# Kernel tuning notes

Hardware: AMD Instinct MI355X
Metric: run time of the kernel (lower is better)

The kernel has to match this reference:

```python
import jax, jax.numpy as jnp
import numpy as np

KEY_DIM = 64
SCALE_PER_SEQ = 1.0 / np.sqrt(KEY_DIM).astype(np.float32)   # attn_scale_factor_per_seq default
SCALE_OVER_SEQS = 1.0 / np.sqrt(KEY_DIM).astype(np.float32) # attn_scale_factor_over_seqs default


def setup_inputs() -> dict:
    key = jax.random.key(0)
    ks = jax.random.split(key, 6)
    b, i, t, j, d = 8, 256, 64, 256, 256
    kd, vd = KEY_DIM, 64
    return {
        "input_seq": jax.random.normal(ks[0], (b, i, d), dtype=jnp.float32),
        "memory_x": jax.random.normal(ks[1], (b, t, j, d), dtype=jnp.float32),
        "memory_y": jax.random.normal(ks[2], (b, t, j, d), dtype=jnp.float32),
        "Wq": jax.random.normal(ks[3], (d, kd), dtype=jnp.float32) * (1.0 / np.sqrt(d)),
        "bq": jnp.zeros((kd,), dtype=jnp.float32),
        "Wk": jax.random.normal(ks[4], (d, kd), dtype=jnp.float32) * (1.0 / np.sqrt(d)),
        "bk": jnp.zeros((kd,), dtype=jnp.float32),
        "Wv": jax.random.normal(ks[5], (d, vd), dtype=jnp.float32) * (1.0 / np.sqrt(d)),
        "bv": jnp.zeros((vd,), dtype=jnp.float32),
    }


def reference(input_seq, memory_x, memory_y, Wq, bq, Wk, bk, Wv, bv):
    # Dense projections
    queries = input_seq @ Wq + bq            # [b, i, kd]
    keys = memory_x @ Wk + bk                # [b, t, j, kd]
    values = memory_y @ Wv + bv              # [b, t, j, vd]

    # Raw scores between every query and every token of every memory sequence
    attn_mat = jnp.einsum('bik,btjk->btij', queries, keys)  # [b, t, i, j]

    # Level 1: within-sequence attention (softmax over tokens j)
    per_seq_attn = jax.nn.softmax(SCALE_PER_SEQ * attn_mat, axis=-1)
    per_seq_retrieved = jnp.einsum('btij,btjk->btik', per_seq_attn, values)  # [b, t, i, vd]

    # Level 2: over-sequences attention (max over j, softmax over t)
    mem_seq_scores = jnp.max(attn_mat, axis=-1)                      # [b, t, i]
    mem_seq_attn = jax.nn.softmax(SCALE_OVER_SEQS * mem_seq_scores, axis=1)

    retrieved_mems = jnp.einsum('bti,btik->bik', mem_seq_attn, per_seq_retrieved)  # [b, i, vd]
    return retrieved_mems
```

## Files before the change

kernel.cpp:

```cpp
#include <hip/hip_runtime.h>
#include <hip/hip_bf16.h>

#define NB 8
#define NT 64
#define NI 256
#define NJ 256
#define ND 256
#define NKD 64
#define NVD 64
#define SCL 0.125f

typedef __attribute__((ext_vector_type(4))) float f32x4;
typedef __attribute__((ext_vector_type(8))) short bf16x8;
typedef __attribute__((ext_vector_type(4))) short bf16x4;
typedef __attribute__((ext_vector_type(4))) unsigned int uint32x4;

#define MFMA16(A, B, C) __builtin_amdgcn_mfma_f32_16x16x32_bf16((A), (B), (C), 0, 0, 0)

#define R2B 32768

__device__ __forceinline__ unsigned short f2bf(float x) {
  return __builtin_bit_cast(unsigned short, __float2bfloat16(x));
}
__device__ __forceinline__ float bf2f(unsigned short h) {
  return __builtin_bit_cast(float, (unsigned)h << 16);
}
__device__ __forceinline__ void split8(const float* __restrict__ x, bf16x8& hi, bf16x8& lo) {
  #pragma unroll
  for (int e = 0; e < 8; ++e) {
    unsigned short h = f2bf(x[e]);
    hi[e] = (short)h;
    lo[e] = (short)f2bf(x[e] - bf2f(h));
  }
}

__global__ __launch_bounds__(256) void k_prep_projq(
    const float* __restrict__ x, const float* __restrict__ Wq,
    const float* __restrict__ bq,
    const float* __restrict__ Wk, const float* __restrict__ Wv,
    unsigned short* __restrict__ Wkth, unsigned short* __restrict__ Wvth,
    unsigned short* __restrict__ Qh) {
  int tid = threadIdx.x;
  if (blockIdx.x >= 128) {
    int t0 = (blockIdx.x - 128) * 2048 + tid * 8;
    #pragma unroll
    for (int e = 0; e < 8; ++e) {
      int t = t0 + e;
      int d = t >> 6, kd = t & 63;
      Wkth[kd * 256 + d] = f2bf(Wk[t]);
      Wvth[kd * 256 + d] = f2bf(Wv[t]);
    }
    return;
  }
  __shared__ __align__(16) float wqs[256 * 64];
  __shared__ __align__(16) float xs[16 * 256];
  #pragma unroll 8
  for (int it = 0; it < 64; ++it)
    wqs[tid + it * 256] = Wq[tid + it * 256];
  int r0 = blockIdx.x * 16;
  #pragma unroll
  for (int it = 0; it < 16; ++it)
    xs[tid + it * 256] = x[(size_t)r0 * 256 + tid + it * 256];
  __syncthreads();
  int kd = tid & 63, rr = tid >> 6;
  #pragma unroll
  for (int rp = 0; rp < 4; ++rp) {
    int r = rp * 4 + rr;
    float a0 = bq[kd], a1 = 0.f, a2 = 0.f, a3 = 0.f;
    #pragma unroll 4
    for (int d = 0; d < 256; d += 4) {
      a0 = fmaf(xs[r * 256 + d],     wqs[(d)     * 64 + kd], a0);
      a1 = fmaf(xs[r * 256 + d + 1], wqs[(d + 1) * 64 + kd], a1);
      a2 = fmaf(xs[r * 256 + d + 2], wqs[(d + 2) * 64 + kd], a2);
      a3 = fmaf(xs[r * 256 + d + 3], wqs[(d + 3) * 64 + kd], a3);
    }
    Qh[(size_t)(r0 + r) * 64 + kd] = f2bf((a0 + a1) + (a2 + a3));
  }
}

__device__ __forceinline__ void stage_plane(
    char* dstb, const unsigned short* __restrict__ Wt, int tid) {
  #pragma unroll
  for (int it = 0; it < 4; ++it) {
    int qq = tid + it * 512;
    int r = qq >> 5, pb = qq & 31;
    uint4 v = *(const uint4*)((const char*)Wt + (size_t)qq * 16);
    *(uint4*)(dstb + r * 512 + ((pb ^ (r & 7)) << 4)) = v;
  }
}

__global__ __launch_bounds__(512, 4) void k_fused(
    const float* __restrict__ Xm, const float* __restrict__ Ym,
    const unsigned short* __restrict__ Wkth, const unsigned short* __restrict__ Wvth,
    const float* __restrict__ bk, const float* __restrict__ bv,
    const unsigned short* __restrict__ Qh,
    unsigned short* __restrict__ R,
    float* __restrict__ Sc) {
  __shared__ __align__(16) char smemb[65536];
  int tid = threadIdx.x;
  int bt = blockIdx.x, b = bt >> 6;
  int w = tid >> 6, lane = tid & 63, c = lane & 15, g = lane >> 4;

  const float* xr0 = Xm + (size_t)bt * 65536 + (size_t)(w * 32 + c) * 256 + g * 8;
  const float* xr1 = xr0 + 16 * 256;
  const float* yr0 = Ym + (size_t)bt * 65536 + (size_t)(w * 32 + c) * 256 + g * 8;
  const float* yr1 = yr0 + 16 * 256;

  float4 xa0 = *(const float4*)(xr0),      xa1 = *(const float4*)(xr0 + 4);
  float4 xa2 = *(const float4*)(xr1),      xa3 = *(const float4*)(xr1 + 4);
  float4 xb0 = *(const float4*)(xr0 + 32), xb1 = *(const float4*)(xr0 + 36);
  float4 xb2 = *(const float4*)(xr1 + 32), xb3 = *(const float4*)(xr1 + 36);
  float4 ya0 = *(const float4*)(yr0),      ya1 = *(const float4*)(yr0 + 4);
  float4 ya2 = *(const float4*)(yr1),      ya3 = *(const float4*)(yr1 + 4);
  float4 yb0 = *(const float4*)(yr0 + 32), yb1 = *(const float4*)(yr0 + 36);
  float4 yb2 = *(const float4*)(yr1 + 32), yb3 = *(const float4*)(yr1 + 36);

  stage_plane(smemb, Wkth, tid);
  stage_plane(smemb + R2B, Wvth, tid);
  __syncthreads();

  f32x4 kacc[4][2];
  f32x4 vacc[2][4];
  #pragma unroll
  for (int mf = 0; mf < 4; ++mf) { kacc[mf][0] = (f32x4)0.f; kacc[mf][1] = (f32x4)0.f; }
  #pragma unroll
  for (int mf = 0; mf < 2; ++mf)
    #pragma unroll
    for (int nf = 0; nf < 4; ++nf) vacc[mf][nf] = (f32x4)0.f;

  #pragma unroll
  for (int ks = 0; ks < 8; ++ks) {
    float x0[8], x1[8];
    if (ks & 1) {
      *(float4*)&x0[0] = xb0; *(float4*)&x0[4] = xb1;
      *(float4*)&x1[0] = xb2; *(float4*)&x1[4] = xb3;
      if (ks < 6) {
        xb0 = *(const float4*)(xr0 + (ks + 2) * 32);
        xb1 = *(const float4*)(xr0 + (ks + 2) * 32 + 4);
        xb2 = *(const float4*)(xr1 + (ks + 2) * 32);
        xb3 = *(const float4*)(xr1 + (ks + 2) * 32 + 4);
      }
    } else {
      *(float4*)&x0[0] = xa0; *(float4*)&x0[4] = xa1;
      *(float4*)&x1[0] = xa2; *(float4*)&x1[4] = xa3;
      if (ks < 6) {
        xa0 = *(const float4*)(xr0 + (ks + 2) * 32);
        xa1 = *(const float4*)(xr0 + (ks + 2) * 32 + 4);
        xa2 = *(const float4*)(xr1 + (ks + 2) * 32);
        xa3 = *(const float4*)(xr1 + (ks + 2) * 32 + 4);
      }
    }
    {
      bf16x8 b0h, b0l, b1h, b1l;
      split8(x0, b0h, b0l);
      split8(x1, b1h, b1l);
      #pragma unroll
      for (int mf = 0; mf < 4; ++mf) {
        int r = mf * 16 + c;
        int ba = r * 512 + (((ks * 4 + g) ^ (r & 7)) << 4);
        bf16x8 awh = *(const bf16x8*)(smemb + ba);
        kacc[mf][0] = MFMA16(awh, b0h, kacc[mf][0]);
        kacc[mf][0] = MFMA16(awh, b0l, kacc[mf][0]);
        kacc[mf][1] = MFMA16(awh, b1h, kacc[mf][1]);
        kacc[mf][1] = MFMA16(awh, b1l, kacc[mf][1]);
      }
    }
    float y0[8], y1[8];
    if (ks & 1) {
      *(float4*)&y0[0] = yb0; *(float4*)&y0[4] = yb1;
      *(float4*)&y1[0] = yb2; *(float4*)&y1[4] = yb3;
      if (ks < 6) {
        yb0 = *(const float4*)(yr0 + (ks + 2) * 32);
        yb1 = *(const float4*)(yr0 + (ks + 2) * 32 + 4);
        yb2 = *(const float4*)(yr1 + (ks + 2) * 32);
        yb3 = *(const float4*)(yr1 + (ks + 2) * 32 + 4);
      }
    } else {
      *(float4*)&y0[0] = ya0; *(float4*)&y0[4] = ya1;
      *(float4*)&y1[0] = ya2; *(float4*)&y1[4] = ya3;
      if (ks < 6) {
        ya0 = *(const float4*)(yr0 + (ks + 2) * 32);
        ya1 = *(const float4*)(yr0 + (ks + 2) * 32 + 4);
        ya2 = *(const float4*)(yr1 + (ks + 2) * 32);
        ya3 = *(const float4*)(yr1 + (ks + 2) * 32 + 4);
      }
    }
    {
      bf16x8 a0h, a0l, a1h, a1l;
      split8(y0, a0h, a0l);
      split8(y1, a1h, a1l);
      #pragma unroll
      for (int nf = 0; nf < 4; ++nf) {
        int r = nf * 16 + c;
        int ba = R2B + r * 512 + (((ks * 4 + g) ^ (r & 7)) << 4);
        bf16x8 bwh = *(const bf16x8*)(smemb + ba);
        vacc[0][nf] = MFMA16(a0h, bwh, vacc[0][nf]);
        vacc[0][nf] = MFMA16(a0l, bwh, vacc[0][nf]);
        vacc[1][nf] = MFMA16(a1h, bwh, vacc[1][nf]);
        vacc[1][nf] = MFMA16(a1l, bwh, vacc[1][nf]);
      }
    }
  }
  bf16x8 qbh[2][2];
  #pragma unroll
  for (int ks = 0; ks < 2; ++ks)
    #pragma unroll
    for (int ic = 0; ic < 2; ++ic) {
      size_t qo = ((size_t)b * NI + w * 32 + ic * 16 + c) * NKD + ks * 32 + g * 8;
      qbh[ks][ic] = *(const bf16x8*)(Qh + qo);
    }
  __syncthreads();

  #pragma unroll
  for (int nf = 0; nf < 2; ++nf) {
    int j = w * 32 + nf * 16 + c;
    #pragma unroll
    for (int mf = 0; mf < 4; ++mf) {
      bf16x4 ph;
      #pragma unroll
      for (int r = 0; r < 4; ++r)
        ph[r] = (short)f2bf(kacc[mf][nf][r] + bk[mf * 16 + g * 4 + r]);
      int pb = mf * 2 + (g >> 1);
      int ba = j * 128 + ((pb ^ (j & 7)) << 4) + (g & 1) * 8;
      *(bf16x4*)(smemb + ba) = ph;
    }
  }
  #pragma unroll
  for (int nf = 0; nf < 4; ++nf) {
    int vd = nf * 16 + c;
    float bs = bv[vd];
    #pragma unroll
    for (int mf = 0; mf < 2; ++mf) {
      bf16x4 ph;
      #pragma unroll
      for (int r = 0; r < 4; ++r) ph[r] = (short)f2bf(vacc[mf][nf][r] + bs);
      int pb = w * 4 + mf * 2 + (g >> 1);
      int ba = R2B + vd * 512 + ((pb ^ (vd & 7)) << 4) + (g & 1) * 8;
      *(bf16x4*)(smemb + ba) = ph;
    }
  }
  __syncthreads();

  #pragma unroll
  for (int ic = 0; ic < 2; ++ic) {
    int i = w * 32 + ic * 16 + c;

    f32x4 sa[16];
    #pragma unroll
    for (int jf = 0; jf < 16; ++jf) sa[jf] = (f32x4)0.f;
    #pragma unroll
    for (int jf = 0; jf < 16; ++jf) {
      int j = jf * 16 + c;
      #pragma unroll
      for (int ks = 0; ks < 2; ++ks) {
        int ba = j * 128 + (((ks * 4 + g) ^ (j & 7)) << 4);
        bf16x8 kh = *(const bf16x8*)(smemb + ba);
        sa[jf] = MFMA16(kh, qbh[ks][ic], sa[jf]);
      }
    }

    float mx = sa[0][0];
    #pragma unroll
    for (int jf = 0; jf < 16; ++jf)
      #pragma unroll
      for (int r = 0; r < 4; ++r) mx = fmaxf(mx, sa[jf][r]);
    mx = fmaxf(mx, __shfl_xor(mx, 16));
    mx = fmaxf(mx, __shfl_xor(mx, 32));
    if (g == 0) Sc[(size_t)bt * NI + i] = mx;
    float sum = 0.f;
    #pragma unroll
    for (int jf = 0; jf < 16; ++jf)
      #pragma unroll
      for (int r = 0; r < 4; ++r) {
        float p = __expf((sa[jf][r] - mx) * SCL);
        sa[jf][r] = p;
        sum += p;
      }
    sum += __shfl_xor(sum, 16);
    sum += __shfl_xor(sum, 32);
    float linv = 1.0f / sum;

    unsigned int plo[16], phi[16];
    #pragma unroll
    for (int jf = 0; jf < 16; ++jf) {
      plo[jf] = (unsigned int)f2bf(sa[jf][0]) | ((unsigned int)f2bf(sa[jf][1]) << 16);
      phi[jf] = (unsigned int)f2bf(sa[jf][2]) | ((unsigned int)f2bf(sa[jf][3]) << 16);
    }

    int srcA = c + 32 * (g & 1);
    int srcB = srcA + 16;
    bool hiH = (g >= 2);

    f32x4 racc[4];
    #pragma unroll
    for (int vf = 0; vf < 4; ++vf) racc[vf] = (f32x4)0.f;
    #pragma unroll
    for (int js = 0; js < 8; ++js) {
      int a0 = __shfl((int)plo[2 * js], srcA);
      int a1 = __shfl((int)phi[2 * js], srcA);
      int a2 = __shfl((int)plo[2 * js], srcB);
      int a3 = __shfl((int)phi[2 * js], srcB);
      int b0 = __shfl((int)plo[2 * js + 1], srcA);
      int b1 = __shfl((int)phi[2 * js + 1], srcA);
      int b2 = __shfl((int)plo[2 * js + 1], srcB);
      int b3 = __shfl((int)phi[2 * js + 1], srcB);
      uint32x4 pw;
      pw[0] = (unsigned int)(hiH ? b0 : a0);
      pw[1] = (unsigned int)(hiH ? b1 : a1);
      pw[2] = (unsigned int)(hiH ? b2 : a2);
      pw[3] = (unsigned int)(hiH ? b3 : a3);
      bf16x8 pf = __builtin_bit_cast(bf16x8, pw);
      #pragma unroll
      for (int vf = 0; vf < 4; ++vf) {
        int vd = vf * 16 + c;
        int vba = R2B + vd * 512 + (((js * 4 + g) ^ (vd & 7)) << 4);
        bf16x8 vh = *(const bf16x8*)(smemb + vba);
        racc[vf] = MFMA16(vh, pf, racc[vf]);
      }
    }

    #pragma unroll
    for (int vf = 0; vf < 4; ++vf) {
      bf16x4 rk;
      #pragma unroll
      for (int r = 0; r < 4; ++r) rk[r] = (short)f2bf(racc[vf][r] * linv);
      *(bf16x4*)(R + ((size_t)bt * NI + i) * NKD + vf * 16 + g * 4) = rk;
    }
  }
}

__global__ __launch_bounds__(256) void k_level2(
    const float* __restrict__ Sc,
    const unsigned short* __restrict__ R,
    float* __restrict__ out) {
  int w = threadIdx.x >> 6, lane = threadIdx.x & 63;
  int bi = blockIdx.x * 4 + w;
  int b = bi >> 8, i = bi & 255;
  float sc = Sc[((size_t)b * NT + lane) * NI + i];
  float mx = sc;
  #pragma unroll
  for (int off = 32; off; off >>= 1) mx = fmaxf(mx, __shfl_xor(mx, off));
  float e = __expf((sc - mx) * SCL);
  float sum = e;
  #pragma unroll
  for (int off = 32; off; off >>= 1) sum += __shfl_xor(sum, off);
  float wn = e / sum;
  float acc = 0.f;
  for (int t = 0; t < NT; ++t) {
    float wt = __shfl(wn, t);
    acc = fmaf(wt, bf2f(R[(((size_t)b * NT + t) * NI + i) * NKD + lane]), acc);
  }
  out[((size_t)b * NI + i) * NVD + lane] = acc;
}

extern "C" void kernel_launch(void* const* d_in, const int* in_sizes, int n_in,
                              void* d_out, int out_size, void* d_ws, size_t ws_size,
                              hipStream_t stream) {
  const float* x   = (const float*)d_in[0];
  const float* mxp = (const float*)d_in[1];
  const float* myp = (const float*)d_in[2];
  const float* Wq  = (const float*)d_in[3];
  const float* bq  = (const float*)d_in[4];
  const float* Wk  = (const float*)d_in[5];
  const float* bk  = (const float*)d_in[6];
  const float* Wv  = (const float*)d_in[7];
  const float* bv  = (const float*)d_in[8];
  float* out = (float*)d_out;

  char* p = (char*)d_ws;
  auto alloc = [&](size_t bytes) { char* r = p; p += (bytes + 255) & ~(size_t)255; return r; };
  unsigned short* Qh   = (unsigned short*)alloc(2048 * 64 * 2);
  unsigned short* Rw   = (unsigned short*)alloc((size_t)131072 * 64 * 2);
  float*          Scw  = (float*)alloc((size_t)131072 * 4);
  unsigned short* Wkth = (unsigned short*)alloc(64 * 256 * 2);
  unsigned short* Wvth = (unsigned short*)alloc(64 * 256 * 2);

  hipLaunchKernelGGL(k_prep_projq, dim3(136), dim3(256), 0, stream,
                     x, Wq, bq, Wk, Wv, Wkth, Wvth, Qh);
  hipLaunchKernelGGL(k_fused, dim3(NB * NT), dim3(512), 0, stream,
                     mxp, myp, Wkth, Wvth, bk, bv, Qh, Rw, Scw);
  hipLaunchKernelGGL(k_level2, dim3(512), dim3(256), 0, stream, Scw, Rw, out);
}
```

Before: 88.90 us.

## Transpose R layout to [b,i,t,vd] and vectorize level-2 reduction over t

The fused kernel now writes the per-sequence retrieved vectors in a [b, i, t, vd] layout, so all 64 memory sequences for one query row sit next to each other. The level-2 kernel splits each wave into 8 groups over t that each load 16-byte vectors, accumulate 8 outputs, and combine the partial sums with xor shuffles. This replaces 64 serial strided scalar loads per lane with a few wide contiguous loads. In exchange, the fused kernel's stores become scattered across t, which may hurt its write coalescing.

```diff
diff --git a/kernel.cpp b/kernel.cpp
--- a/kernel.cpp
+++ b/kernel.cpp
@@ -98,7 +98,7 @@
     float* __restrict__ Sc) {
   __shared__ __align__(16) char smemb[65536];
   int tid = threadIdx.x;
-  int bt = blockIdx.x, b = bt >> 6;
+  int bt = blockIdx.x, b = bt >> 6, tmem = bt & 63;
   int w = tid >> 6, lane = tid & 63, c = lane & 15, g = lane >> 4;
 
   const float* xr0 = Xm + (size_t)bt * 65536 + (size_t)(w * 32 + c) * 256 + g * 8;
@@ -324,7 +324,7 @@
       bf16x4 rk;
       #pragma unroll
       for (int r = 0; r < 4; ++r) rk[r] = (short)f2bf(racc[vf][r] * linv);
-      *(bf16x4*)(R + ((size_t)bt * NI + i) * NKD + vf * 16 + g * 4) = rk;
+      *(bf16x4*)(R + (((size_t)b * NI + i) * NT + tmem) * NKD + vf * 16 + g * 4) = rk;
     }
   }
 }
@@ -345,12 +345,33 @@
   #pragma unroll
   for (int off = 32; off; off >>= 1) sum += __shfl_xor(sum, off);
   float wn = e / sum;
-  float acc = 0.f;
-  for (int t = 0; t < NT; ++t) {
+  int tg = lane >> 3, vg = lane & 7;
+  const unsigned short* rb = R + ((size_t)b * NI + i) * (NT * NKD);
+  float acc[8];
+  #pragma unroll
+  for (int v8 = 0; v8 < 8; ++v8) acc[v8] = 0.f;
+  #pragma unroll
+  for (int tt = 0; tt < 8; ++tt) {
+    int t = tg * 8 + tt;
     float wt = __shfl(wn, t);
-    acc = fmaf(wt, bf2f(R[(((size_t)b * NT + t) * NI + i) * NKD + lane]), acc);
-  }
-  out[((size_t)b * NI + i) * NVD + lane] = acc;
+    uint4 rv = *(const uint4*)(rb + (size_t)t * NKD + vg * 8);
+    const unsigned short* rs = (const unsigned short*)&rv;
+    #pragma unroll
+    for (int v8 = 0; v8 < 8; ++v8) acc[v8] = fmaf(wt, bf2f(rs[v8]), acc[v8]);
+  }
+  #pragma unroll
+  for (int v8 = 0; v8 < 8; ++v8) {
+    float v = acc[v8];
+    v += __shfl_xor(v, 8);
+    v += __shfl_xor(v, 16);
+    v += __shfl_xor(v, 32);
+    acc[v8] = v;
+  }
+  if (tg == 0) {
+    float* op = out + ((size_t)b * NI + i) * NVD + vg * 8;
+    #pragma unroll
+    for (int v8 = 0; v8 < 8; ++v8) op[v8] = acc[v8];
+  }
 }
 
 extern "C" void kernel_launch(void* const* d_in, const int* in_sizes, int n_in,
```

Result: faster. 85.99 us (-3.3%).
